# Kernel tuning notes

Hardware: AMD Instinct MI355X
Metric: run time of the kernel (lower is better)

Reference implementation:

```python
import jax, jax.numpy as jnp
import numpy as np

PARENTS = [-1, 0, 0, 0, 1, 2, 3, 4, 5, 6, 7, 8, 9, 9, 9, 12, 13, 14, 16, 17, 18, 19]
NUM_JOINTS = 22
EPS = 1e-12  # matches F.normalize eps


def _cont6d_to_mat(d6):
    """6D rotation rep -> 3x3 rotation matrix (columns b1,b2,b3)."""
    a1, a2 = d6[..., :3], d6[..., 3:]
    b1 = a1 / jnp.maximum(jnp.linalg.norm(a1, axis=-1, keepdims=True), EPS)
    b2 = a2 - b1 * jnp.sum(b1 * a2, axis=-1, keepdims=True)
    b2 = b2 / jnp.maximum(jnp.linalg.norm(b2, axis=-1, keepdims=True), EPS)
    b3 = jnp.cross(b1, b2)
    return jnp.stack((b1, b2, b3), axis=-1)  # [..., 3, 3]


def setup_inputs() -> dict:
    key = jax.random.key(0)
    k1, k2, k3 = jax.random.split(key, 3)
    B, S = 32, 4096
    pred_pos = jax.random.normal(k1, (B, S, 20, 3), dtype=jnp.float32)
    gt_rot = jax.random.normal(k2, (B, S, NUM_JOINTS, 6), dtype=jnp.float32)
    offsets = jax.random.normal(k3, (NUM_JOINTS, 3), dtype=jnp.float32) * 0.2
    return {"pred_pos": pred_pos, "gt_rot": gt_rot, "offsets": offsets}


def reference(pred_pos, gt_rot, offsets):
    B, S = gt_rot.shape[:2]
    dtype = gt_rot.dtype
    rot_mats = _cont6d_to_mat(gt_rot)  # [B,S,22,3,3]
    eye = jnp.broadcast_to(jnp.eye(3, dtype=dtype), (B, S, 3, 3))

    g_rot = [None] * NUM_JOINTS
    g_pos = [None] * NUM_JOINTS
    # Root and joint 1 rotations forced to identity (canonical frame).
    g_rot[0] = eye
    g_pos[0] = jnp.zeros((B, S, 3), dtype=dtype)
    # Sequential FK chain over the fixed 22-joint tree.
    for i in range(1, NUM_JOINTS):
        p = PARENTS[i]
        local_rot = eye if i == 1 else rot_mats[:, :, i]
        g_rot[i] = jnp.einsum('bsij,bsjk->bsik', g_rot[p], local_rot)
        g_pos[i] = g_pos[p] + jnp.einsum('bsij,j->bsi', g_rot[p], offsets[i])

    gt_pos = jnp.stack(g_pos[2:NUM_JOINTS], axis=2)  # [B,S,20,3]
    dist = jnp.linalg.norm(pred_pos - gt_pos, axis=-1)  # [B,S,20]
    mpjpe_mm = dist.mean() * 1000.0
    return mpjpe_mm
```

## Files before the change

### kernel.cpp

```cpp
#include <hip/hip_runtime.h>

#define NJ 22

__device__ __forceinline__ void rot6d_to_mat(float a1x, float a1y, float a1z,
                                             float a2x, float a2y, float a2z,
                                             float* R) {
    float n1 = sqrtf(a1x * a1x + a1y * a1y + a1z * a1z);
    float inv1 = 1.0f / fmaxf(n1, 1e-12f);
    float b1x = a1x * inv1, b1y = a1y * inv1, b1z = a1z * inv1;
    float d = b1x * a2x + b1y * a2y + b1z * a2z;
    float b2x = a2x - b1x * d, b2y = a2y - b1y * d, b2z = a2z - b1z * d;
    float n2 = sqrtf(b2x * b2x + b2y * b2y + b2z * b2z);
    float inv2 = 1.0f / fmaxf(n2, 1e-12f);
    b2x *= inv2; b2y *= inv2; b2z *= inv2;
    float b3x = b1y * b2z - b1z * b2y;
    float b3y = b1z * b2x - b1x * b2z;
    float b3z = b1x * b2y - b1y * b2x;
    R[0] = b1x; R[1] = b2x; R[2] = b3x;
    R[3] = b1y; R[4] = b2y; R[5] = b3y;
    R[6] = b1z; R[7] = b2z; R[8] = b3z;
}

__device__ __forceinline__ void matmul3(const float* __restrict__ A,
                                        const float* __restrict__ B,
                                        float* __restrict__ C) {
#pragma unroll
    for (int r = 0; r < 3; ++r) {
#pragma unroll
        for (int c = 0; c < 3; ++c) {
            C[r * 3 + c] = A[r * 3 + 0] * B[0 * 3 + c]
                         + A[r * 3 + 1] * B[1 * 3 + c]
                         + A[r * 3 + 2] * B[2 * 3 + c];
        }
    }
}

__global__ __launch_bounds__(256, 1) void mpjpe_fk_kernel(
    const float4* __restrict__ pred4,
    const float4* __restrict__ rot4,
    const float* __restrict__ offsets,
    float* __restrict__ out,
    int nposes, float scale)
{
    constexpr int PAR[NJ] = {-1, 0, 0, 0, 1, 2, 3, 4, 5, 6, 7, 8, 9, 9, 9, 12, 13, 14, 16, 17, 18, 19};

    int t = blockIdx.x * blockDim.x + threadIdx.x;
    float sum = 0.0f;

    if (t < nposes) {
        float rf[120];
        float pf[60];
        const float4* gp = rot4 + (size_t)t * 33 + 3;
        const float4* pp = pred4 + (size_t)t * 15;
#pragma unroll
        for (int k = 0; k < 30; ++k) {
            float4 v = gp[k];
            rf[4*k+0] = v.x; rf[4*k+1] = v.y; rf[4*k+2] = v.z; rf[4*k+3] = v.w;
        }
#pragma unroll
        for (int k = 0; k < 15; ++k) {
            float4 v = pp[k];
            pf[4*k+0] = v.x; pf[4*k+1] = v.y; pf[4*k+2] = v.z; pf[4*k+3] = v.w;
        }

        float R[NJ][9];
        float P[NJ][3];

        R[0][0] = 1.f; R[0][1] = 0.f; R[0][2] = 0.f;
        R[0][3] = 0.f; R[0][4] = 1.f; R[0][5] = 0.f;
        R[0][6] = 0.f; R[0][7] = 0.f; R[0][8] = 1.f;
        P[0][0] = 0.f; P[0][1] = 0.f; P[0][2] = 0.f;

#pragma unroll
        for (int i = 1; i < NJ; ++i) {
            const int p = PAR[i];
            float ox = offsets[i * 3 + 0];
            float oy = offsets[i * 3 + 1];
            float oz = offsets[i * 3 + 2];
#pragma unroll
            for (int r = 0; r < 3; ++r) {
                P[i][r] = P[p][r] + R[p][r * 3 + 0] * ox
                                  + R[p][r * 3 + 1] * oy
                                  + R[p][r * 3 + 2] * oz;
            }
            if (i == 1) {
#pragma unroll
                for (int k = 0; k < 9; ++k) R[i][k] = R[p][k];
            } else {
                const int r0 = 6 * i - 12;
                float M[9];
                rot6d_to_mat(rf[r0+0], rf[r0+1], rf[r0+2],
                             rf[r0+3], rf[r0+4], rf[r0+5], M);
                matmul3(R[p], M, R[i]);
            }
            if (i >= 2) {
                const int q0 = 3 * i - 6;
                float dx = pf[q0+0] - P[i][0];
                float dy = pf[q0+1] - P[i][1];
                float dz = pf[q0+2] - P[i][2];
                sum += sqrtf(dx * dx + dy * dy + dz * dz);
            }
        }
    }

#pragma unroll
    for (int o = 32; o > 0; o >>= 1) sum += __shfl_down(sum, o, 64);

    __shared__ float ws[4];
    int lane = threadIdx.x & 63;
    int wid = threadIdx.x >> 6;
    if (lane == 0) ws[wid] = sum;
    __syncthreads();
    if (threadIdx.x == 0) {
        float s = ws[0] + ws[1] + ws[2] + ws[3];
        atomicAdd(out, s * scale);
    }
}

extern "C" void kernel_launch(void* const* d_in, const int* in_sizes, int n_in,
                              void* d_out, int out_size, void* d_ws, size_t ws_size,
                              hipStream_t stream) {
    const float4* pred4 = (const float4*)d_in[0];
    const float4* rot4  = (const float4*)d_in[1];
    const float* offsets = (const float*)d_in[2];
    float* out = (float*)d_out;

    int nposes = in_sizes[1] / (NJ * 6);
    float scale = 1000.0f / ((float)nposes * 20.0f);

    hipMemsetAsync(out, 0, sizeof(float), stream);

    int block = 256;
    int grid = (nposes + block - 1) / block;
    mpjpe_fk_kernel<<<grid, block, 0, stream>>>(pred4, rot4, offsets, out, nposes, scale);
}
```

Before: 137.7 us.

## Stage rotation data through LDS with coalesced loads and smaller blocks

```diff
diff --git a/kernel.cpp b/kernel.cpp
--- a/kernel.cpp
+++ b/kernel.cpp
@@ -1,6 +1,8 @@
 #include <hip/hip_runtime.h>
 
 #define NJ 22
+#define TILE 128
+#define PW 121
 
 __device__ __forceinline__ void rot6d_to_mat(float a1x, float a1y, float a1z,
                                              float a2x, float a2y, float a2z,
@@ -35,7 +37,7 @@
     }
 }
 
-__global__ __launch_bounds__(256, 1) void mpjpe_fk_kernel(
+__global__ __launch_bounds__(128) void mpjpe_fk_kernel(
     const float4* __restrict__ pred4,
     const float4* __restrict__ rot4,
     const float* __restrict__ offsets,
@@ -44,24 +46,39 @@
 {
     constexpr int PAR[NJ] = {-1, 0, 0, 0, 1, 2, 3, 4, 5, 6, 7, 8, 9, 9, 9, 12, 13, 14, 16, 17, 18, 19};
 
-    int t = blockIdx.x * blockDim.x + threadIdx.x;
-    float sum = 0.0f;
+    __shared__ float lds[TILE * PW];
+    __shared__ float ws[2];
 
-    if (t < nposes) {
-        float rf[120];
-        float pf[60];
-        const float4* gp = rot4 + (size_t)t * 33 + 3;
-        const float4* pp = pred4 + (size_t)t * 15;
-#pragma unroll
-        for (int k = 0; k < 30; ++k) {
-            float4 v = gp[k];
-            rf[4*k+0] = v.x; rf[4*k+1] = v.y; rf[4*k+2] = v.z; rf[4*k+3] = v.w;
-        }
+    const int tid  = threadIdx.x;
+    const int base = blockIdx.x * TILE;
+    const int pose = base + tid;
+
+    float pf[60];
+    if (pose < nposes) {
+        const float4* pp = pred4 + (size_t)pose * 15;
 #pragma unroll
         for (int k = 0; k < 15; ++k) {
             float4 v = pp[k];
             pf[4*k+0] = v.x; pf[4*k+1] = v.y; pf[4*k+2] = v.z; pf[4*k+3] = v.w;
         }
+    }
+
+#pragma unroll
+    for (int j = 0; j < 30; ++j) {
+        int n = j * TILE + tid;
+        int p = n / 30;
+        int q = n - p * 30;
+        if (base + p < nposes) {
+            float4 v = rot4[(size_t)(base + p) * 33 + 3 + q];
+            float* dst = &lds[p * PW + q * 4];
+            dst[0] = v.x; dst[1] = v.y; dst[2] = v.z; dst[3] = v.w;
+        }
+    }
+    __syncthreads();
+
+    float sum = 0.0f;
+    if (pose < nposes) {
+        const float* rec = &lds[tid * PW];
 
         float R[NJ][9];
         float P[NJ][3];
@@ -87,14 +104,14 @@
 #pragma unroll
                 for (int k = 0; k < 9; ++k) R[i][k] = R[p][k];
             } else {
-                const int r0 = 6 * i - 12;
+                const int r0 = 6 * (i - 2);
                 float M[9];
-                rot6d_to_mat(rf[r0+0], rf[r0+1], rf[r0+2],
-                             rf[r0+3], rf[r0+4], rf[r0+5], M);
+                rot6d_to_mat(rec[r0+0], rec[r0+1], rec[r0+2],
+                             rec[r0+3], rec[r0+4], rec[r0+5], M);
                 matmul3(R[p], M, R[i]);
             }
             if (i >= 2) {
-                const int q0 = 3 * i - 6;
+                const int q0 = 3 * (i - 2);
                 float dx = pf[q0+0] - P[i][0];
                 float dy = pf[q0+1] - P[i][1];
                 float dz = pf[q0+2] - P[i][2];
@@ -106,14 +123,12 @@
 #pragma unroll
     for (int o = 32; o > 0; o >>= 1) sum += __shfl_down(sum, o, 64);
 
-    __shared__ float ws[4];
-    int lane = threadIdx.x & 63;
-    int wid = threadIdx.x >> 6;
+    const int lane = tid & 63;
+    const int wid  = tid >> 6;
     if (lane == 0) ws[wid] = sum;
     __syncthreads();
-    if (threadIdx.x == 0) {
-        float s = ws[0] + ws[1] + ws[2] + ws[3];
-        atomicAdd(out, s * scale);
+    if (tid == 0) {
+        atomicAdd(out, (ws[0] + ws[1]) * scale);
     }
 }
 
@@ -130,7 +145,6 @@
 
     hipMemsetAsync(out, 0, sizeof(float), stream);
 
-    int block = 256;
-    int grid = (nposes + block - 1) / block;
-    mpjpe_fk_kernel<<<grid, block, 0, stream>>>(pred4, rot4, offsets, out, nposes, scale);
+    int grid = (nposes + TILE - 1) / TILE;
+    mpjpe_fk_kernel<<<grid, 128, 0, stream>>>(pred4, rot4, offsets, out, nposes, scale);
 }
```

New measurement: 153.2 us. +11.2%, slower.
